# Kernel tuning notes

Hardware: AMD Instinct MI355X
Metric: run time of the kernel (lower is better)

## Reference

```python
import jax, jax.numpy as jnp
import numpy as np

DIM = 256
HEADS = 8
HEAD_DIM = DIM // HEADS
B, N = 32, 8192


def setup_inputs() -> dict:
    key = jax.random.key(0)
    ks = jax.random.split(key, 12)
    s = 0.02
    return {
        "inputs": jax.random.normal(ks[0], (B, N, DIM), jnp.float32),
        "class_token": jax.random.normal(ks[1], (B, 1, DIM), jnp.float32),
        "mask": jax.random.randint(ks[2], (B, 1, N), 0, 2, jnp.int32),
        "W_kv": jax.random.normal(ks[3], (DIM, 2 * DIM), jnp.float32) * s,
        "b_kv": jnp.zeros((2 * DIM,), jnp.float32),
        "W_q": jax.random.normal(ks[4], (DIM, DIM), jnp.float32) * s,
        "b_q": jnp.zeros((DIM,), jnp.float32),
        "W_t1": jax.random.normal(ks[5], (HEADS, HEADS), jnp.float32) * 0.3,
        "b_t1": jnp.zeros((HEADS,), jnp.float32),
        "W_t2": jax.random.normal(ks[6], (HEADS, HEADS), jnp.float32) * 0.3,
        "b_t2": jnp.zeros((HEADS,), jnp.float32),
        "W_out": jax.random.normal(ks[7], (DIM, DIM), jnp.float32) * s,
        "b_out": jnp.zeros((DIM,), jnp.float32),
    }


def reference(inputs, class_token, mask, W_kv, b_kv, W_q, b_q, W_t1, b_t1, W_t2, b_t2, W_out, b_out):
    b, n, c = inputs.shape
    h, hd = HEADS, HEAD_DIM
    # K, V projections: (B,N,2C) -> (B,N,2,H,hd)
    kv = (inputs @ W_kv + b_kv).reshape(b, n, 2, h, hd)
    k = kv[:, :, 0]  # (B,N,H,hd)
    v = kv[:, :, 1]  # (B,N,H,hd)
    # Single query from class token: (B,1,C) -> (B,H,1,hd)
    q = (class_token @ W_q + b_q).reshape(b, h, 1, hd)
    # Scaled scores: (B,H,1,N)
    scores = jnp.einsum("bhqd,bnhd->bhqn", q, k) / jnp.sqrt(jnp.float32(hd))
    # Talking heads (pre-softmax): mix across head axis
    scores = jnp.einsum("bhqn,hg->bgqn", scores, W_t1) + b_t1[None, :, None, None]
    # Keras Softmax(mask): add large negative to masked positions
    m = mask.astype(scores.dtype)[:, None]  # (B,1,1,N)
    scores = scores + (1.0 - m) * (-1e9)
    attn = jax.nn.softmax(scores, axis=-1)
    # Talking heads (post-softmax)
    attn = jnp.einsum("bhqn,hg->bgqn", attn, W_t2) + b_t2[None, :, None, None]
    # Attend values: (B,H,1,hd) -> (B,1,C)
    out = jnp.einsum("bhqn,bnhd->bhqd", attn, v)
    out = out.transpose(0, 2, 1, 3).reshape(b, 1, c)
    return out @ W_out + b_out
```

## Files before the change

kernel.cpp:

```cpp
#include <hip/hip_runtime.h>

#define TDIM 256
#define THEADS 8
#define TB 32
#define TN 8192
#define NPAIR (TN/2)
#define BLK_PER_B 16
#define WAVES_PB 4
#define GW_PER_B (BLK_PER_B*WAVES_PB)
#define ITERS (NPAIR/GW_PER_B)
#define ACC_PER_B 2312

__device__ __forceinline__ float xr(float v, int m) { return v + __shfl_xor(v, m, 64); }

__global__ void tmca_zero(float* __restrict__ acc, int n) {
  int i = blockIdx.x * 256 + threadIdx.x;
  if (i < n) acc[i] = 0.0f;
}

__global__ void tmca_qproj(const float* __restrict__ ct, const float* __restrict__ Wq,
                           const float* __restrict__ bq, float* __restrict__ q) {
  int b = blockIdx.x, t = threadIdx.x;
  __shared__ float s[TDIM];
  s[t] = ct[b * TDIM + t];
  __syncthreads();
  float a = bq[t];
  for (int c = 0; c < TDIM; ++c) a = fmaf(s[c], Wq[c * TDIM + t], a);
  q[b * TDIM + t] = a;
}

__global__ void tmca_w1(const float* __restrict__ q, const float* __restrict__ Wkv,
                        const float* __restrict__ Wt1, float* __restrict__ w1) {
  int b = blockIdx.x, c = threadIdx.x;
  __shared__ float sq[TDIM];
  __shared__ float st1[THEADS * THEADS];
  sq[c] = q[b * TDIM + c];
  if (c < THEADS * THEADS) st1[c] = Wt1[c];
  __syncthreads();
  float ph[THEADS];
  #pragma unroll
  for (int h = 0; h < THEADS; ++h) {
    float a = 0.0f;
    #pragma unroll 8
    for (int d = 0; d < 32; ++d) a = fmaf(Wkv[c * 512 + h * 32 + d], sq[h * 32 + d], a);
    ph[h] = a;
  }
  const float inv = 0.17677669529663687f;
  #pragma unroll
  for (int g = 0; g < THEADS; ++g) {
    float a = 0.0f;
    #pragma unroll
    for (int h = 0; h < THEADS; ++h) a = fmaf(ph[h], st1[h * THEADS + g], a);
    w1[(b * THEADS + g) * TDIM + c] = a * inv;
  }
}

__global__ __launch_bounds__(256, 2) void tmca_main(
    const float* __restrict__ X, const int* __restrict__ mask,
    const float* __restrict__ w1, float* __restrict__ acc) {
  const int b = blockIdx.y;
  const int bk = blockIdx.x;
  const int tid = threadIdx.x;
  const int wv = tid >> 6;
  const int lane = tid & 63;
  const int half = lane >> 5;
  const int j = lane & 31;
  const int gw = bk * WAVES_PB + wv;

  const float4* w1b = (const float4*)(w1 + (size_t)b * THEADS * TDIM);
  float4 wg0[8], wg1[8];
  #pragma unroll
  for (int g = 0; g < 8; ++g) {
    wg0[g] = w1b[g * 64 + j];
    wg1[g] = w1b[g * 64 + 32 + j];
  }

  float4 Y0[8], Y1[8];
  float E[8];
  float4 S0 = make_float4(0, 0, 0, 0), S1 = make_float4(0, 0, 0, 0);
  #pragma unroll
  for (int g = 0; g < 8; ++g) {
    Y0[g] = make_float4(0, 0, 0, 0);
    Y1[g] = make_float4(0, 0, 0, 0);
    E[g] = 0.0f;
  }

  const float4* Xb = (const float4*)(X + (size_t)b * TN * TDIM);
  const int* mb = mask + b * TN;

  int p = gw;
  int n0 = 2 * p + half;
  float4 a0 = Xb[(size_t)n0 * 64 + j];
  float4 a1 = Xb[(size_t)n0 * 64 + 32 + j];
  int mk = mb[n0];

  for (int it = 0; it < ITERS; ++it) {
    float4 x0 = a0, x1 = a1;
    float fm = (float)mk;
    if (it + 1 < ITERS) {
      int n2 = 2 * (p + GW_PER_B) + half;
      a0 = Xb[(size_t)n2 * 64 + j];
      a1 = Xb[(size_t)n2 * 64 + 32 + j];
      mk = mb[n2];
    }
    p += GW_PER_B;

    float pg[8];
    #pragma unroll
    for (int g = 0; g < 8; ++g) {
      pg[g] = x0.x * wg0[g].x + x0.y * wg0[g].y + x0.z * wg0[g].z + x0.w * wg0[g].w
            + x1.x * wg1[g].x + x1.y * wg1[g].y + x1.z * wg1[g].z + x1.w * wg1[g].w;
    }
    #pragma unroll
    for (int st = 1; st <= 16; st <<= 1) {
      #pragma unroll
      for (int g = 0; g < 8; ++g) pg[g] += __shfl_xor(pg[g], st, 64);
    }
    #pragma unroll
    for (int g = 0; g < 8; ++g) {
      float e = __expf(pg[g]) * fm;
      E[g] += e;
      Y0[g].x = fmaf(e, x0.x, Y0[g].x);
      Y0[g].y = fmaf(e, x0.y, Y0[g].y);
      Y0[g].z = fmaf(e, x0.z, Y0[g].z);
      Y0[g].w = fmaf(e, x0.w, Y0[g].w);
      Y1[g].x = fmaf(e, x1.x, Y1[g].x);
      Y1[g].y = fmaf(e, x1.y, Y1[g].y);
      Y1[g].z = fmaf(e, x1.z, Y1[g].z);
      Y1[g].w = fmaf(e, x1.w, Y1[g].w);
    }
    S0.x += x0.x; S0.y += x0.y; S0.z += x0.z; S0.w += x0.w;
    S1.x += x1.x; S1.y += x1.y; S1.z += x1.z; S1.w += x1.w;
  }

  #pragma unroll
  for (int g = 0; g < 8; ++g) {
    Y0[g].x = xr(Y0[g].x, 32); Y0[g].y = xr(Y0[g].y, 32);
    Y0[g].z = xr(Y0[g].z, 32); Y0[g].w = xr(Y0[g].w, 32);
    Y1[g].x = xr(Y1[g].x, 32); Y1[g].y = xr(Y1[g].y, 32);
    Y1[g].z = xr(Y1[g].z, 32); Y1[g].w = xr(Y1[g].w, 32);
    E[g] = xr(E[g], 32);
  }
  S0.x = xr(S0.x, 32); S0.y = xr(S0.y, 32); S0.z = xr(S0.z, 32); S0.w = xr(S0.w, 32);
  S1.x = xr(S1.x, 32); S1.y = xr(S1.y, 32); S1.z = xr(S1.z, 32); S1.w = xr(S1.w, 32);

  __shared__ float red[WAVES_PB][ACC_PER_B];
  float* sl = red[wv];
  if (lane < 32) {
    #pragma unroll
    for (int g = 0; g < 8; ++g) {
      ((float4*)(sl + g * TDIM))[j] = Y0[g];
      ((float4*)(sl + g * TDIM + 128))[j] = Y1[g];
    }
    ((float4*)(sl + 2056))[j] = S0;
    ((float4*)(sl + 2056 + 128))[j] = S1;
    if (lane == 0) {
      #pragma unroll
      for (int g = 0; g < 8; ++g) sl[2048 + g] = E[g];
    }
  }
  __syncthreads();
  float* gb = acc + b * ACC_PER_B;
  for (int idx = tid; idx < ACC_PER_B; idx += 256) {
    float v = red[0][idx] + red[1][idx] + red[2][idx] + red[3][idx];
    atomicAdd(gb + idx, v);
  }
}

__global__ void tmca_fin(const float* __restrict__ acc, const float* __restrict__ Wkv,
                         const float* __restrict__ bkv, const float* __restrict__ Wt2,
                         const float* __restrict__ bt2, const float* __restrict__ Wout,
                         const float* __restrict__ bout, float* __restrict__ out) {
  int b = blockIdx.x, t = threadIdx.x;
  __shared__ float z[THEADS][TDIM];
  __shared__ float opre[TDIM];
  __shared__ float sWt2[THEADS * THEADS];
  __shared__ float sE[THEADS];
  __shared__ float sbt2[THEADS];
  const float* ab = acc + b * ACC_PER_B;
  if (t < THEADS * THEADS) sWt2[t] = Wt2[t];
  if (t < THEADS) { sE[t] = ab[2048 + t]; sbt2[t] = bt2[t]; }
  __syncthreads();
  float Yc[THEADS];
  #pragma unroll
  for (int g = 0; g < THEADS; ++g) Yc[g] = ab[g * TDIM + t] / sE[g];
  float Sc = ab[2056 + t];
  #pragma unroll
  for (int g2 = 0; g2 < THEADS; ++g2) {
    float a = 0.0f;
    #pragma unroll
    for (int g = 0; g < THEADS; ++g) a = fmaf(sWt2[g * THEADS + g2], Yc[g], a);
    z[g2][t] = a + sbt2[g2] * Sc;
  }
  __syncthreads();
  {
    int g2 = t >> 5;
    float T = 0.0f;
    #pragma unroll
    for (int g = 0; g < THEADS; ++g) T += sWt2[g * THEADS + g2];
    T += (float)TN * sbt2[g2];
    float a = 0.0f;
    for (int c = 0; c < TDIM; ++c) a = fmaf(z[g2][c], Wkv[c * 512 + 256 + t], a);
    opre[t] = a + T * bkv[256 + t];
  }
  __syncthreads();
  float a = bout[t];
  for (int c = 0; c < TDIM; ++c) a = fmaf(opre[c], Wout[c * TDIM + t], a);
  out[b * TDIM + t] = a;
}

extern "C" void kernel_launch(void* const* d_in, const int* in_sizes, int n_in,
                              void* d_out, int out_size, void* d_ws, size_t ws_size,
                              hipStream_t stream) {
  const float* X    = (const float*)d_in[0];
  const float* ct   = (const float*)d_in[1];
  const int*   msk  = (const int*)d_in[2];
  const float* Wkv  = (const float*)d_in[3];
  const float* bkv  = (const float*)d_in[4];
  const float* Wq   = (const float*)d_in[5];
  const float* bq   = (const float*)d_in[6];
  const float* Wt1  = (const float*)d_in[7];
  const float* Wt2  = (const float*)d_in[9];
  const float* bt2  = (const float*)d_in[10];
  const float* Wout = (const float*)d_in[11];
  const float* bout = (const float*)d_in[12];
  float* out = (float*)d_out;

  float* ws  = (float*)d_ws;
  float* q   = ws;
  float* w1  = ws + 8192;
  float* acc = ws + 8192 + 65536;
  const int accN = TB * ACC_PER_B;

  hipLaunchKernelGGL(tmca_zero, dim3((accN + 255) / 256), dim3(256), 0, stream, acc, accN);
  hipLaunchKernelGGL(tmca_qproj, dim3(TB), dim3(256), 0, stream, ct, Wq, bq, q);
  hipLaunchKernelGGL(tmca_w1, dim3(TB), dim3(256), 0, stream, q, Wkv, Wt1, w1);
  hipLaunchKernelGGL(tmca_main, dim3(BLK_PER_B, TB), dim3(256), 0, stream, X, msk, w1, acc);
  hipLaunchKernelGGL(tmca_fin, dim3(TB), dim3(256), 0, stream, acc, Wkv, bkv, Wt2, bt2,
                     Wout, bout, out);
}
```

Baseline: 426.9 us.

## Fuse prep kernels, deepen prefetch, DPP reductions, exp2, drop atomics

Merges the q-projection and w1 kernels into one prep kernel and removes the zeroing kernel by writing per-block partials that the final kernel sums in shared memory, instead of using global atomics. The main loop now prefetches two iterations ahead with a manually unrolled A/B pipeline. It replaces shfl_xor reductions with DPP and ds_swizzle steps and uses exp2 with log2(e) folded into w1. The aim is to cut launch count, atomic traffic and per-iteration shuffle/latency cost, at the price of more registers and an extra partial buffer read in the finalizer.

Result: no change. 431.5 us (+1.1%).

```diff
diff --git a/kernel.cpp b/kernel.cpp
--- a/kernel.cpp
+++ b/kernel.cpp
@@ -10,70 +10,74 @@
 #define GW_PER_B (BLK_PER_B*WAVES_PB)
 #define ITERS (NPAIR/GW_PER_B)
 #define ACC_PER_B 2312
+#define PPAD 2368
+
+#if __has_builtin(__builtin_amdgcn_exp2f)
+#define EXP2(x) __builtin_amdgcn_exp2f(x)
+#else
+#define EXP2(x) exp2f(x)
+#endif
 
 __device__ __forceinline__ float xr(float v, int m) { return v + __shfl_xor(v, m, 64); }
 
-__global__ void tmca_zero(float* __restrict__ acc, int n) {
-  int i = blockIdx.x * 256 + threadIdx.x;
-  if (i < n) acc[i] = 0.0f;
-}
-
-__global__ void tmca_qproj(const float* __restrict__ ct, const float* __restrict__ Wq,
-                           const float* __restrict__ bq, float* __restrict__ q) {
+template<int CTRL>
+__device__ __forceinline__ float dppadd(float v) {
+  int t = __builtin_amdgcn_update_dpp(0, __float_as_int(v), CTRL, 0xF, 0xF, true);
+  return v + __int_as_float(t);
+}
+__device__ __forceinline__ float swzadd16(float v) {
+  int t = __builtin_amdgcn_ds_swizzle(__float_as_int(v), 0x401F);
+  return v + __int_as_float(t);
+}
+__device__ __forceinline__ float red32(float v) {
+  v = dppadd<0xB1>(v);
+  v = dppadd<0x4E>(v);
+  v = dppadd<0x141>(v);
+  v = dppadd<0x128>(v);
+  return swzadd16(v);
+}
+
+__global__ void tmca_prep(const float* __restrict__ ct, const float* __restrict__ Wq,
+                          const float* __restrict__ bq, const float* __restrict__ Wkv,
+                          const float* __restrict__ Wt1, float* __restrict__ w1) {
   int b = blockIdx.x, t = threadIdx.x;
-  __shared__ float s[TDIM];
-  s[t] = ct[b * TDIM + t];
+  __shared__ float sct[TDIM], sq[TDIM], st1[64];
+  sct[t] = ct[b * TDIM + t];
+  if (t < 64) st1[t] = Wt1[t];
   __syncthreads();
   float a = bq[t];
-  for (int c = 0; c < TDIM; ++c) a = fmaf(s[c], Wq[c * TDIM + t], a);
-  q[b * TDIM + t] = a;
-}
-
-__global__ void tmca_w1(const float* __restrict__ q, const float* __restrict__ Wkv,
-                        const float* __restrict__ Wt1, float* __restrict__ w1) {
-  int b = blockIdx.x, c = threadIdx.x;
-  __shared__ float sq[TDIM];
-  __shared__ float st1[THEADS * THEADS];
-  sq[c] = q[b * TDIM + c];
-  if (c < THEADS * THEADS) st1[c] = Wt1[c];
+  for (int c = 0; c < TDIM; ++c) a = fmaf(sct[c], Wq[c * TDIM + t], a);
+  sq[t] = a;
   __syncthreads();
   float ph[THEADS];
   #pragma unroll
   for (int h = 0; h < THEADS; ++h) {
-    float a = 0.0f;
+    float s = 0.f;
     #pragma unroll 8
-    for (int d = 0; d < 32; ++d) a = fmaf(Wkv[c * 512 + h * 32 + d], sq[h * 32 + d], a);
-    ph[h] = a;
-  }
-  const float inv = 0.17677669529663687f;
+    for (int d = 0; d < 32; ++d) s = fmaf(Wkv[t * 512 + h * 32 + d], sq[h * 32 + d], s);
+    ph[h] = s;
+  }
+  const float sc = 0.17677669529663687f * 1.4426950408889634f;
   #pragma unroll
   for (int g = 0; g < THEADS; ++g) {
-    float a = 0.0f;
-    #pragma unroll
-    for (int h = 0; h < THEADS; ++h) a = fmaf(ph[h], st1[h * THEADS + g], a);
-    w1[(b * THEADS + g) * TDIM + c] = a * inv;
+    float s = 0.f;
+    #pragma unroll
+    for (int h = 0; h < THEADS; ++h) s = fmaf(ph[h], st1[h * THEADS + g], s);
+    w1[(b * THEADS + g) * TDIM + t] = s * sc;
   }
 }
 
 __global__ __launch_bounds__(256, 2) void tmca_main(
     const float* __restrict__ X, const int* __restrict__ mask,
-    const float* __restrict__ w1, float* __restrict__ acc) {
-  const int b = blockIdx.y;
-  const int bk = blockIdx.x;
-  const int tid = threadIdx.x;
-  const int wv = tid >> 6;
-  const int lane = tid & 63;
-  const int half = lane >> 5;
-  const int j = lane & 31;
+    const float* __restrict__ w1, float* __restrict__ partial) {
+  const int b = blockIdx.y, bk = blockIdx.x, tid = threadIdx.x;
+  const int wv = tid >> 6, lane = tid & 63, half = lane >> 5, j = lane & 31;
   const int gw = bk * WAVES_PB + wv;
 
   const float4* w1b = (const float4*)(w1 + (size_t)b * THEADS * TDIM);
   float4 wg0[8], wg1[8];
   #pragma unroll
-  for (int g = 0; g < 8; ++g) {
-    wg0[g] = w1b[g * 64 + j];
-    wg1[g] = w1b[g * 64 + 32 + j];
-  }
+  for (int g = 0; g < 8; ++g) { wg0[g] = w1b[g * 64 + j]; wg1[g] = w1b[g * 64 + 32 + j]; }
 
   float4 Y0[8], Y1[8];
   float E[8];
@@ -82,43 +86,30 @@
   for (int g = 0; g < 8; ++g) {
     Y0[g] = make_float4(0, 0, 0, 0);
     Y1[g] = make_float4(0, 0, 0, 0);
-    E[g] = 0.0f;
+    E[g] = 0.f;
   }
 
   const float4* Xb = (const float4*)(X + (size_t)b * TN * TDIM);
   const int* mb = mask + b * TN;
-
-  int p = gw;
-  int n0 = 2 * p + half;
-  float4 a0 = Xb[(size_t)n0 * 64 + j];
-  float4 a1 = Xb[(size_t)n0 * 64 + 32 + j];
-  int mk = mb[n0];
-
-  for (int it = 0; it < ITERS; ++it) {
-    float4 x0 = a0, x1 = a1;
+  const int n0 = 2 * gw + half;
+
+  float4 A0 = Xb[(size_t)n0 * 64 + j], A1 = Xb[(size_t)n0 * 64 + 32 + j];
+  int mA = mb[n0];
+  float4 B0 = Xb[(size_t)(n0 + 128) * 64 + j], B1 = Xb[(size_t)(n0 + 128) * 64 + 32 + j];
+  int mB = mb[n0 + 128];
+
+  auto body = [&](float4 x0, float4 x1, int mk) {
     float fm = (float)mk;
-    if (it + 1 < ITERS) {
-      int n2 = 2 * (p + GW_PER_B) + half;
-      a0 = Xb[(size_t)n2 * 64 + j];
-      a1 = Xb[(size_t)n2 * 64 + 32 + j];
-      mk = mb[n2];
-    }
-    p += GW_PER_B;
-
     float pg[8];
     #pragma unroll
-    for (int g = 0; g < 8; ++g) {
+    for (int g = 0; g < 8; ++g)
       pg[g] = x0.x * wg0[g].x + x0.y * wg0[g].y + x0.z * wg0[g].z + x0.w * wg0[g].w
             + x1.x * wg1[g].x + x1.y * wg1[g].y + x1.z * wg1[g].z + x1.w * wg1[g].w;
-    }
-    #pragma unroll
-    for (int st = 1; st <= 16; st <<= 1) {
-      #pragma unroll
-      for (int g = 0; g < 8; ++g) pg[g] += __shfl_xor(pg[g], st, 64);
-    }
+    #pragma unroll
+    for (int g = 0; g < 8; ++g) pg[g] = red32(pg[g]);
     #pragma unroll
     for (int g = 0; g < 8; ++g) {
-      float e = __expf(pg[g]) * fm;
+      float e = EXP2(pg[g]) * fm;
       E[g] += e;
       Y0[g].x = fmaf(e, x0.x, Y0[g].x);
       Y0[g].y = fmaf(e, x0.y, Y0[g].y);
@@ -131,7 +122,24 @@
     }
     S0.x += x0.x; S0.y += x0.y; S0.z += x0.z; S0.w += x0.w;
     S1.x += x1.x; S1.y += x1.y; S1.z += x1.z; S1.w += x1.w;
-  }
+  };
+
+  for (int it = 0; it < ITERS - 2; it += 2) {
+    {
+      float4 x0 = A0, x1 = A1; int mk = mA;
+      int nn = n0 + 128 * (it + 2);
+      A0 = Xb[(size_t)nn * 64 + j]; A1 = Xb[(size_t)nn * 64 + 32 + j]; mA = mb[nn];
+      body(x0, x1, mk);
+    }
+    {
+      float4 x0 = B0, x1 = B1; int mk = mB;
+      int nn = n0 + 128 * (it + 3);
+      B0 = Xb[(size_t)nn * 64 + j]; B1 = Xb[(size_t)nn * 64 + 32 + j]; mB = mb[nn];
+      body(x0, x1, mk);
+    }
+  }
+  body(A0, A1, mA);
+  body(B0, B1, mB);
 
   #pragma unroll
   for (int g = 0; g < 8; ++g) {
@@ -160,34 +168,37 @@
     }
   }
   __syncthreads();
-  float* gb = acc + b * ACC_PER_B;
-  for (int idx = tid; idx < ACC_PER_B; idx += 256) {
-    float v = red[0][idx] + red[1][idx] + red[2][idx] + red[3][idx];
-    atomicAdd(gb + idx, v);
-  }
-}
-
-__global__ void tmca_fin(const float* __restrict__ acc, const float* __restrict__ Wkv,
+  float* pb = partial + (size_t)(b * BLK_PER_B + bk) * PPAD;
+  for (int idx = tid; idx < ACC_PER_B; idx += 256)
+    pb[idx] = red[0][idx] + red[1][idx] + red[2][idx] + red[3][idx];
+}
+
+__global__ void tmca_fin(const float* __restrict__ partial, const float* __restrict__ Wkv,
                          const float* __restrict__ bkv, const float* __restrict__ Wt2,
                          const float* __restrict__ bt2, const float* __restrict__ Wout,
                          const float* __restrict__ bout, float* __restrict__ out) {
   int b = blockIdx.x, t = threadIdx.x;
+  __shared__ float sacc[ACC_PER_B];
   __shared__ float z[THEADS][TDIM];
   __shared__ float opre[TDIM];
-  __shared__ float sWt2[THEADS * THEADS];
-  __shared__ float sE[THEADS];
-  __shared__ float sbt2[THEADS];
-  const float* ab = acc + b * ACC_PER_B;
-  if (t < THEADS * THEADS) sWt2[t] = Wt2[t];
-  if (t < THEADS) { sE[t] = ab[2048 + t]; sbt2[t] = bt2[t]; }
+  __shared__ float sWt2[64], sbt2[8];
+  const float* pb = partial + (size_t)b * BLK_PER_B * PPAD;
+  for (int idx = t; idx < ACC_PER_B; idx += 256) {
+    float s = 0.f;
+    #pragma unroll
+    for (int k = 0; k < BLK_PER_B; ++k) s += pb[(size_t)k * PPAD + idx];
+    sacc[idx] = s;
+  }
+  if (t < 64) sWt2[t] = Wt2[t];
+  if (t < 8) sbt2[t] = bt2[t];
   __syncthreads();
   float Yc[THEADS];
   #pragma unroll
-  for (int g = 0; g < THEADS; ++g) Yc[g] = ab[g * TDIM + t] / sE[g];
-  float Sc = ab[2056 + t];
+  for (int g = 0; g < THEADS; ++g) Yc[g] = sacc[g * TDIM + t] / sacc[2048 + g];
+  float Sc = sacc[2056 + t];
   #pragma unroll
   for (int g2 = 0; g2 < THEADS; ++g2) {
-    float a = 0.0f;
+    float a = 0.f;
     #pragma unroll
     for (int g = 0; g < THEADS; ++g) a = fmaf(sWt2[g * THEADS + g2], Yc[g], a);
     z[g2][t] = a + sbt2[g2] * Sc;
@@ -195,11 +206,11 @@
   __syncthreads();
   {
     int g2 = t >> 5;
-    float T = 0.0f;
+    float T = 0.f;
     #pragma unroll
     for (int g = 0; g < THEADS; ++g) T += sWt2[g * THEADS + g2];
     T += (float)TN * sbt2[g2];
-    float a = 0.0f;
+    float a = 0.f;
     for (int c = 0; c < TDIM; ++c) a = fmaf(z[g2][c], Wkv[c * 512 + 256 + t], a);
     opre[t] = a + T * bkv[256 + t];
   }
@@ -226,16 +237,12 @@
   const float* bout = (const float*)d_in[12];
   float* out = (float*)d_out;
 
-  float* ws  = (float*)d_ws;
-  float* q   = ws;
-  float* w1  = ws + 8192;
-  float* acc = ws + 8192 + 65536;
-  const int accN = TB * ACC_PER_B;
-
-  hipLaunchKernelGGL(tmca_zero, dim3((accN + 255) / 256), dim3(256), 0, stream, acc, accN);
-  hipLaunchKernelGGL(tmca_qproj, dim3(TB), dim3(256), 0, stream, ct, Wq, bq, q);
-  hipLaunchKernelGGL(tmca_w1, dim3(TB), dim3(256), 0, stream, q, Wkv, Wt1, w1);
-  hipLaunchKernelGGL(tmca_main, dim3(BLK_PER_B, TB), dim3(256), 0, stream, X, msk, w1, acc);
-  hipLaunchKernelGGL(tmca_fin, dim3(TB), dim3(256), 0, stream, acc, Wkv, bkv, Wt2, bt2,
+  float* ws      = (float*)d_ws;
+  float* w1      = ws;
+  float* partial = ws + TB * THEADS * TDIM;
+
+  hipLaunchKernelGGL(tmca_prep, dim3(TB), dim3(256), 0, stream, ct, Wq, bq, Wkv, Wt1, w1);
+  hipLaunchKernelGGL(tmca_main, dim3(BLK_PER_B, TB), dim3(256), 0, stream, X, msk, w1, partial);
+  hipLaunchKernelGGL(tmca_fin, dim3(TB), dim3(256), 0, stream, partial, Wkv, bkv, Wt2, bt2,
                      Wout, bout, out);
 }
```
